# Optimization experiments

Measured on AMD Instinct MI355X. Metric: run time of the kernel, lower is better.

Reference implementation:

```python
import jax, jax.numpy as jnp
import numpy as np

MODEL_DIM = 4096
NUM_EXPERTS = 64
TOPK = 2
ROUTE_SCALE = 1.0


def setup_inputs() -> dict:
    key = jax.random.key(0)
    kx, kw = jax.random.split(key)
    x = jax.random.normal(kx, (16384, MODEL_DIM), dtype=jnp.float32)
    # xavier_uniform for [num_experts, model_dim]
    limit = float(np.sqrt(6.0 / (NUM_EXPERTS + MODEL_DIM)))
    weight = jax.random.uniform(kw, (NUM_EXPERTS, MODEL_DIM), dtype=jnp.float32,
                                minval=-limit, maxval=limit)
    return {"x": x, "weight": weight}


def reference(x, weight):
    # scores: [N, num_experts]
    scores = jnp.einsum('nd,ed->ne', x, weight)
    all_scores = jax.nn.softmax(scores, axis=-1)  # score_func='softmax'
    topk_vals, topk_idx = jax.lax.top_k(all_scores, TOPK)  # [N, topk]
    topk_vals = topk_vals * ROUTE_SCALE
    return (topk_vals, topk_idx, all_scores)
```

## Files before the change

kernel.cpp:

```cpp
#include <hip/hip_runtime.h>
#include <math.h>

#define N_ROWS 16384
#define DIM 4096
#define NEXP 64
#define KWAVES 16
#define KSLICE (DIM / KWAVES)
#define KC 32
#define NCHUNK (KSLICE / KC)
#define RPB 32
#define NKO (DIM / 8)

typedef short short8 __attribute__((ext_vector_type(8)));
typedef float f32x4  __attribute__((ext_vector_type(4)));

__device__ __forceinline__ unsigned cvt_pk_bf16(float a, float b) {
    unsigned r;
    asm("v_cvt_pk_bf16_f32 %0, %1, %2" : "=v"(r) : "v"(a), "v"(b));
    return r;
}

__device__ __forceinline__ void split3(const float* xv, short8& h8, short8& m8, short8& l8) {
    union { unsigned u[4]; short8 s; } H, M, L;
#pragma unroll
    for (int j = 0; j < 4; ++j) {
        float a = xv[2 * j], b = xv[2 * j + 1];
        unsigned hp = cvt_pk_bf16(a, b);
        float a1 = a - __uint_as_float(hp << 16);
        float b1 = b - __uint_as_float(hp & 0xffff0000u);
        unsigned mp = cvt_pk_bf16(a1, b1);
        float a2 = a1 - __uint_as_float(mp << 16);
        float b2 = b1 - __uint_as_float(mp & 0xffff0000u);
        H.u[j] = hp; M.u[j] = mp; L.u[j] = cvt_pk_bf16(a2, b2);
    }
    h8 = H.s; m8 = M.s; l8 = L.s;
}

__device__ __forceinline__ bool gtpair(float a, int ia, float b, int ib) {
    return (a > b) || (a == b && ia < ib);
}

__global__ __launch_bounds__(256)
void convw_kernel(const float* __restrict__ w, short8* __restrict__ w0t,
                  short8* __restrict__ w1t, short8* __restrict__ w2t)
{
    const int t  = blockIdx.x * 256 + threadIdx.x;
    const int ko = t >> 6;
    const int e  = t & 63;
    const float* src = w + (size_t)e * DIM + ko * 8;
    float xv[8];
#pragma unroll
    for (int j = 0; j < 8; ++j) xv[j] = src[j];
    short8 h, m, l;
    split3(xv, h, m, l);
    w0t[ko * 64 + e] = h;
    w1t[ko * 64 + e] = m;
    w2t[ko * 64 + e] = l;
}

__global__ __launch_bounds__(1024, 4)
void gate_kernel(const float* __restrict__ x, const short8* __restrict__ w0t,
                 const short8* __restrict__ w1t, const short8* __restrict__ w2t,
                 float* __restrict__ out)
{
    __shared__ float part[8][RPB][NEXP];

    const int tid  = threadIdx.x;
    const int lane = tid & 63;
    const int wv   = tid >> 6;
    const int l15  = lane & 15;
    const int g    = lane >> 4;
    const int row0 = blockIdx.x * RPB;

    f32x4 acc[2][4];
#pragma unroll
    for (int mt = 0; mt < 2; ++mt)
#pragma unroll
        for (int nt = 0; nt < 4; ++nt) acc[mt][nt] = (f32x4){0.f, 0.f, 0.f, 0.f};

    const float* xp0 = x + (size_t)(row0 + l15) * DIM + wv * KSLICE + g * 8;
    const float* xp1 = xp0 + 16 * DIM;

    float4 c00 = *reinterpret_cast<const float4*>(xp0);
    float4 c01 = *reinterpret_cast<const float4*>(xp0 + 4);
    float4 c10 = *reinterpret_cast<const float4*>(xp1);
    float4 c11 = *reinterpret_cast<const float4*>(xp1 + 4);

    for (int t = 0; t < NCHUNK; ++t) {
        const int base = (wv * 32 + t * 4 + g) * 64 + l15;
        short8 b0[4], b1[4], b2[4];
#pragma unroll
        for (int nt = 0; nt < 4; ++nt) {
            b0[nt] = w0t[base + nt * 16];
            b1[nt] = w1t[base + nt * 16];
            b2[nt] = w2t[base + nt * 16];
        }
        const int tn = (t < NCHUNK - 1 ? t + 1 : t) * KC;
        float4 n00 = *reinterpret_cast<const float4*>(xp0 + tn);
        float4 n01 = *reinterpret_cast<const float4*>(xp0 + tn + 4);
        float4 n10 = *reinterpret_cast<const float4*>(xp1 + tn);
        float4 n11 = *reinterpret_cast<const float4*>(xp1 + tn + 4);

        float v0[8] = {c00.x, c00.y, c00.z, c00.w, c01.x, c01.y, c01.z, c01.w};
        float v1[8] = {c10.x, c10.y, c10.z, c10.w, c11.x, c11.y, c11.z, c11.w};
        short8 a0h, a0m, a0l, a1h, a1m, a1l;
        split3(v0, a0h, a0m, a0l);
        split3(v1, a1h, a1m, a1l);

#pragma unroll
        for (int nt = 0; nt < 4; ++nt) {
            acc[0][nt] = __builtin_amdgcn_mfma_f32_16x16x32_bf16(a0l, b0[nt], acc[0][nt], 0, 0, 0);
            acc[0][nt] = __builtin_amdgcn_mfma_f32_16x16x32_bf16(a0m, b1[nt], acc[0][nt], 0, 0, 0);
            acc[0][nt] = __builtin_amdgcn_mfma_f32_16x16x32_bf16(a0h, b2[nt], acc[0][nt], 0, 0, 0);
            acc[0][nt] = __builtin_amdgcn_mfma_f32_16x16x32_bf16(a0m, b0[nt], acc[0][nt], 0, 0, 0);
            acc[0][nt] = __builtin_amdgcn_mfma_f32_16x16x32_bf16(a0h, b1[nt], acc[0][nt], 0, 0, 0);
            acc[0][nt] = __builtin_amdgcn_mfma_f32_16x16x32_bf16(a0h, b0[nt], acc[0][nt], 0, 0, 0);

            acc[1][nt] = __builtin_amdgcn_mfma_f32_16x16x32_bf16(a1l, b0[nt], acc[1][nt], 0, 0, 0);
            acc[1][nt] = __builtin_amdgcn_mfma_f32_16x16x32_bf16(a1m, b1[nt], acc[1][nt], 0, 0, 0);
            acc[1][nt] = __builtin_amdgcn_mfma_f32_16x16x32_bf16(a1h, b2[nt], acc[1][nt], 0, 0, 0);
            acc[1][nt] = __builtin_amdgcn_mfma_f32_16x16x32_bf16(a1m, b0[nt], acc[1][nt], 0, 0, 0);
            acc[1][nt] = __builtin_amdgcn_mfma_f32_16x16x32_bf16(a1h, b1[nt], acc[1][nt], 0, 0, 0);
            acc[1][nt] = __builtin_amdgcn_mfma_f32_16x16x32_bf16(a1h, b0[nt], acc[1][nt], 0, 0, 0);
        }
        c00 = n00; c01 = n01; c10 = n10; c11 = n11;
    }

    if (wv >= 8) {
#pragma unroll
        for (int mt = 0; mt < 2; ++mt)
#pragma unroll
            for (int nt = 0; nt < 4; ++nt)
#pragma unroll
                for (int r = 0; r < 4; ++r) {
                    const int rw = mt * 16 + g * 4 + r;
                    const int cl = (nt * 16 + l15) ^ (((rw >> 2) & 3) << 4);
                    part[wv - 8][rw][cl] = acc[mt][nt][r];
                }
    }
    __syncthreads();
    if (wv < 8) {
#pragma unroll
        for (int mt = 0; mt < 2; ++mt)
#pragma unroll
            for (int nt = 0; nt < 4; ++nt)
#pragma unroll
                for (int r = 0; r < 4; ++r) {
                    const int rw = mt * 16 + g * 4 + r;
                    const int cl = (nt * 16 + l15) ^ (((rw >> 2) & 3) << 4);
                    part[wv][rw][cl] += acc[mt][nt][r];
                }
    }
    __syncthreads();

    float* out_vals = out;
    float* out_idx  = out + (size_t)N_ROWS * 2;
    float* out_sc   = out + (size_t)N_ROWS * 4;

#pragma unroll
    for (int i = 0; i < 2; ++i) {
        const int r = wv * 2 + i;
        const int row = row0 + r;
        const int cl = lane ^ (((r >> 2) & 3) << 4);
        float s = 0.f;
#pragma unroll
        for (int kw = 0; kw < 8; ++kw) s += part[kw][r][cl];
        float m = s;
#pragma unroll
        for (int off = 32; off; off >>= 1) m = fmaxf(m, __shfl_xor(m, off));
        float e = expf(s - m);
        float sum = e;
#pragma unroll
        for (int off = 32; off; off >>= 1) sum += __shfl_xor(sum, off);
        float p = e / sum;
        out_sc[(size_t)row * 64 + lane] = p;

        float v1 = p; int i1 = lane; float v2 = -1.f; int i2 = lane;
#pragma unroll
        for (int off = 32; off; off >>= 1) {
            float o1 = __shfl_xor(v1, off); int oi1 = __shfl_xor(i1, off);
            float o2 = __shfl_xor(v2, off); int oi2 = __shfl_xor(i2, off);
            if (gtpair(o1, oi1, v1, i1)) {
                if (gtpair(v1, i1, o2, oi2)) { v2 = v1; i2 = i1; }
                else                         { v2 = o2; i2 = oi2; }
                v1 = o1; i1 = oi1;
            } else if (gtpair(o1, oi1, v2, i2)) {
                v2 = o1; i2 = oi1;
            }
        }
        if (lane == 0) {
            out_vals[(size_t)row * 2 + 0] = v1;
            out_vals[(size_t)row * 2 + 1] = v2;
            out_idx[(size_t)row * 2 + 0]  = (float)i1;
            out_idx[(size_t)row * 2 + 1]  = (float)i2;
        }
    }
}

extern "C" void kernel_launch(void* const* d_in, const int* in_sizes, int n_in,
                              void* d_out, int out_size, void* d_ws, size_t ws_size,
                              hipStream_t stream)
{
    const float* x = (const float*)d_in[0];
    const float* w = (const float*)d_in[1];
    float* out = (float*)d_out;

    short8* w0t = (short8*)d_ws;
    short8* w1t = w0t + NKO * NEXP;
    short8* w2t = w1t + NKO * NEXP;

    convw_kernel<<<dim3(128), dim3(256), 0, stream>>>(w, w0t, w1t, w2t);
    gate_kernel<<<dim3(N_ROWS / RPB), dim3(1024), 0, stream>>>(x, w0t, w1t, w2t, out);
}
```

Baseline: 92.84 us.

## Halve K-split waves, deepen x prefetch to two chunks, raise MFMA priority

Splits the K dimension across 8 waves instead of 16, giving 512-thread blocks that each walk twice as many chunks. The single-pass LDS reduction replaces the two-phase store/accumulate, and each wave now handles softmax/top-k for 4 rows. The loop is fully unrolled with a two-chunk-deep register prefetch of x, and s_setprio wraps the MFMA block so matrix work is favoured. The aim is to hide global load latency and cut reduction and sync overhead. The cost is fewer waves per block for latency hiding and higher register pressure.

```diff
diff --git a/kernel.cpp b/kernel.cpp
--- a/kernel.cpp
+++ b/kernel.cpp
@@ -4,7 +4,7 @@
 #define N_ROWS 16384
 #define DIM 4096
 #define NEXP 64
-#define KWAVES 16
+#define KWAVES 8
 #define KSLICE (DIM / KWAVES)
 #define KC 32
 #define NCHUNK (KSLICE / KC)
@@ -58,12 +58,12 @@
     w2t[ko * 64 + e] = l;
 }
 
-__global__ __launch_bounds__(1024, 4)
+__global__ __launch_bounds__(512, 4)
 void gate_kernel(const float* __restrict__ x, const short8* __restrict__ w0t,
                  const short8* __restrict__ w1t, const short8* __restrict__ w2t,
                  float* __restrict__ out)
 {
-    __shared__ float part[8][RPB][NEXP];
+    __shared__ float part[KWAVES][RPB][NEXP];
 
     const int tid  = threadIdx.x;
     const int lane = tid & 63;
@@ -81,13 +81,17 @@
     const float* xp0 = x + (size_t)(row0 + l15) * DIM + wv * KSLICE + g * 8;
     const float* xp1 = xp0 + 16 * DIM;
 
-    float4 c00 = *reinterpret_cast<const float4*>(xp0);
-    float4 c01 = *reinterpret_cast<const float4*>(xp0 + 4);
-    float4 c10 = *reinterpret_cast<const float4*>(xp1);
-    float4 c11 = *reinterpret_cast<const float4*>(xp1 + 4);
-
+#define LD4(P) (*reinterpret_cast<const float4*>(P))
+
+    float4 c00 = LD4(xp0),      c01 = LD4(xp0 + 4);
+    float4 c10 = LD4(xp1),      c11 = LD4(xp1 + 4);
+    float4 n00 = LD4(xp0 + 32), n01 = LD4(xp0 + 36);
+    float4 n10 = LD4(xp1 + 32), n11 = LD4(xp1 + 36);
+    float4 f00, f01, f10, f11;
+
+#pragma unroll
     for (int t = 0; t < NCHUNK; ++t) {
-        const int base = (wv * 32 + t * 4 + g) * 64 + l15;
+        const int base = (wv * 64 + t * 4 + g) * 64 + l15;
         short8 b0[4], b1[4], b2[4];
 #pragma unroll
         for (int nt = 0; nt < 4; ++nt) {
@@ -95,11 +99,9 @@
             b1[nt] = w1t[base + nt * 16];
             b2[nt] = w2t[base + nt * 16];
         }
-        const int tn = (t < NCHUNK - 1 ? t + 1 : t) * KC;
-        float4 n00 = *reinterpret_cast<const float4*>(xp0 + tn);
-        float4 n01 = *reinterpret_cast<const float4*>(xp0 + tn + 4);
-        float4 n10 = *reinterpret_cast<const float4*>(xp1 + tn);
-        float4 n11 = *reinterpret_cast<const float4*>(xp1 + tn + 4);
+        const int tcf = (t + 2 < NCHUNK ? t + 2 : NCHUNK - 1) * KC;
+        f00 = LD4(xp0 + tcf);      f01 = LD4(xp0 + tcf + 4);
+        f10 = LD4(xp1 + tcf);      f11 = LD4(xp1 + tcf + 4);
 
         float v0[8] = {c00.x, c00.y, c00.z, c00.w, c01.x, c01.y, c01.z, c01.w};
         float v1[8] = {c10.x, c10.y, c10.z, c10.w, c11.x, c11.y, c11.z, c11.w};
@@ -107,6 +109,7 @@
         split3(v0, a0h, a0m, a0l);
         split3(v1, a1h, a1m, a1l);
 
+        __builtin_amdgcn_s_setprio(1);
 #pragma unroll
         for (int nt = 0; nt < 4; ++nt) {
             acc[0][nt] = __builtin_amdgcn_mfma_f32_16x16x32_bf16(a0l, b0[nt], acc[0][nt], 0, 0, 0);
@@ -123,34 +126,22 @@
             acc[1][nt] = __builtin_amdgcn_mfma_f32_16x16x32_bf16(a1h, b1[nt], acc[1][nt], 0, 0, 0);
             acc[1][nt] = __builtin_amdgcn_mfma_f32_16x16x32_bf16(a1h, b0[nt], acc[1][nt], 0, 0, 0);
         }
+        __builtin_amdgcn_s_setprio(0);
+
         c00 = n00; c01 = n01; c10 = n10; c11 = n11;
+        n00 = f00; n01 = f01; n10 = f10; n11 = f11;
     }
 
-    if (wv >= 8) {
-#pragma unroll
-        for (int mt = 0; mt < 2; ++mt)
-#pragma unroll
-            for (int nt = 0; nt < 4; ++nt)
-#pragma unroll
-                for (int r = 0; r < 4; ++r) {
-                    const int rw = mt * 16 + g * 4 + r;
-                    const int cl = (nt * 16 + l15) ^ (((rw >> 2) & 3) << 4);
-                    part[wv - 8][rw][cl] = acc[mt][nt][r];
-                }
-    }
-    __syncthreads();
-    if (wv < 8) {
-#pragma unroll
-        for (int mt = 0; mt < 2; ++mt)
-#pragma unroll
-            for (int nt = 0; nt < 4; ++nt)
-#pragma unroll
-                for (int r = 0; r < 4; ++r) {
-                    const int rw = mt * 16 + g * 4 + r;
-                    const int cl = (nt * 16 + l15) ^ (((rw >> 2) & 3) << 4);
-                    part[wv][rw][cl] += acc[mt][nt][r];
-                }
-    }
+#pragma unroll
+    for (int mt = 0; mt < 2; ++mt)
+#pragma unroll
+        for (int nt = 0; nt < 4; ++nt)
+#pragma unroll
+            for (int r = 0; r < 4; ++r) {
+                const int rw = mt * 16 + g * 4 + r;
+                const int cl = (nt * 16 + l15) ^ (((rw >> 2) & 3) << 4);
+                part[wv][rw][cl] = acc[mt][nt][r];
+            }
     __syncthreads();
 
     float* out_vals = out;
@@ -158,13 +149,13 @@
     float* out_sc   = out + (size_t)N_ROWS * 4;
 
 #pragma unroll
-    for (int i = 0; i < 2; ++i) {
-        const int r = wv * 2 + i;
+    for (int i = 0; i < 4; ++i) {
+        const int r = wv * 4 + i;
         const int row = row0 + r;
         const int cl = lane ^ (((r >> 2) & 3) << 4);
         float s = 0.f;
 #pragma unroll
-        for (int kw = 0; kw < 8; ++kw) s += part[kw][r][cl];
+        for (int kw = 0; kw < KWAVES; ++kw) s += part[kw][r][cl];
         float m = s;
 #pragma unroll
         for (int off = 32; off; off >>= 1) m = fmaxf(m, __shfl_xor(m, off));
@@ -210,5 +201,5 @@
     short8* w2t = w1t + NKO * NEXP;
 
     convw_kernel<<<dim3(128), dim3(256), 0, stream>>>(w, w0t, w1t, w2t);
-    gate_kernel<<<dim3(N_ROWS / RPB), dim3(1024), 0, stream>>>(x, w0t, w1t, w2t, out);
-}
+    gate_kernel<<<dim3(N_ROWS / RPB), dim3(512), 0, stream>>>(x, w0t, w1t, w2t, out);
+}
```

New measurement: 200.2 us. +115.7%, slower.
